# Performance work log

Measured on AMD Instinct MI355X. Metric: run time of the kernel, lower is better.

## Reference

```python
import jax, jax.numpy as jnp
import numpy as np


def setup_inputs() -> dict:
    key = jax.random.key(0)
    k1, k2 = jax.random.split(key)
    B, V = 8192, 32000
    outputs = jax.random.normal(k1, (B, V), dtype=jnp.float32)
    targets = jax.random.randint(k2, (B,), 0, V, dtype=jnp.int64)
    return {"outputs": outputs, "targets": targets}


def reference(outputs, targets):
    # stable log-softmax over vocab, then gather target log-prob per row
    logp = jax.nn.log_softmax(outputs, axis=-1)          # [B, V]
    picked = jnp.take_along_axis(logp, targets[:, None], axis=-1)[:, 0]  # [B]
    return -jnp.mean(picked)
```

## Files before the change

kernel.cpp:

```cpp
#include <hip/hip_runtime.h>
#include <math.h>


#define LOG2E 1.4426950408889634f
#define LN2   0.6931471805599453f

__global__ __launch_bounds__(256) void ce_row_kernel(const float* __restrict__ x,
                                                     const int* __restrict__ tgt,
                                                     float* __restrict__ row_loss,
                                                     int V) {
    const int row = blockIdx.x;
    const float* xr = x + (size_t)row * (size_t)V;
    const int tid = threadIdx.x;

    float m = -INFINITY;
    float s = 0.0f;
    const int nvec = V >> 2;
    const float4* __restrict__ xv = (const float4*)xr;

    for (int i = tid; i < nvec; i += 256) {
        float4 v = xv[i];
        float vm = fmaxf(fmaxf(v.x, v.y), fmaxf(v.z, v.w));
        float mn = fmaxf(m, vm);
        s = s * exp2f((m - mn) * LOG2E)
          + exp2f((v.x - mn) * LOG2E)
          + exp2f((v.y - mn) * LOG2E)
          + exp2f((v.z - mn) * LOG2E)
          + exp2f((v.w - mn) * LOG2E);
        m = mn;
    }

    #pragma unroll
    for (int off = 1; off < 64; off <<= 1) {
        float om = __shfl_xor(m, off);
        float os = __shfl_xor(s, off);
        float mn = fmaxf(m, om);
        s = s * exp2f((m - mn) * LOG2E) + os * exp2f((om - mn) * LOG2E);
        m = mn;
    }

    __shared__ float sm[4], ss[4];
    const int wave = tid >> 6;
    if ((tid & 63) == 0) { sm[wave] = m; ss[wave] = s; }
    __syncthreads();

    if (tid == 0) {
        float M = sm[0], S = ss[0];
        #pragma unroll
        for (int w = 1; w < 4; ++w) {
            float om = sm[w], os = ss[w];
            float mn = fmaxf(M, om);
            S = S * exp2f((M - mn) * LOG2E) + os * exp2f((om - mn) * LOG2E);
            M = mn;
        }
        float lse = M + log2f(S) * LN2;
        int t = tgt[row];
        row_loss[row] = lse - xr[t];
    }
}

__global__ __launch_bounds__(256) void ce_reduce_kernel(const float* __restrict__ row_loss,
                                                        float* __restrict__ out, int B) {
    float acc = 0.0f;
    for (int i = threadIdx.x; i < B; i += 256) acc += row_loss[i];
    #pragma unroll
    for (int off = 1; off < 64; off <<= 1) acc += __shfl_xor(acc, off);
    __shared__ float sa[4];
    if ((threadIdx.x & 63) == 0) sa[threadIdx.x >> 6] = acc;
    __syncthreads();
    if (threadIdx.x == 0) out[0] = (sa[0] + sa[1] + sa[2] + sa[3]) / (float)B;
}

extern "C" void kernel_launch(void* const* d_in, const int* in_sizes, int n_in,
                              void* d_out, int out_size, void* d_ws, size_t ws_size,
                              hipStream_t stream) {
    const float* x = (const float*)d_in[0];
    const int* tgt = (const int*)d_in[1];
    float* out = (float*)d_out;
    float* ws = (float*)d_ws;

    const int B = in_sizes[1];
    const int V = in_sizes[0] / B;

    ce_row_kernel<<<B, 256, 0, stream>>>(x, tgt, ws, V);
    ce_reduce_kernel<<<1, 256, 0, stream>>>(ws, out, B);
}
```

Before: 194.0 us.

## Map one wavefront per row and keep four independent online-softmax accumulators

```diff
diff --git a/kernel.cpp b/kernel.cpp
--- a/kernel.cpp
+++ b/kernel.cpp
@@ -8,54 +8,50 @@
 __global__ __launch_bounds__(256) void ce_row_kernel(const float* __restrict__ x,
                                                      const int* __restrict__ tgt,
                                                      float* __restrict__ row_loss,
-                                                     int V) {
-    const int row = blockIdx.x;
-    const float* xr = x + (size_t)row * (size_t)V;
-    const int tid = threadIdx.x;
+                                                     int V, int B) {
+    const int wave = threadIdx.x >> 6;
+    const int lane = threadIdx.x & 63;
+    const int row  = (blockIdx.x << 2) + wave;
+    if (row >= B) return;
 
-    float m = -INFINITY;
-    float s = 0.0f;
+    const float* __restrict__ xr = x + (size_t)row * (size_t)V;
+    const float4* __restrict__ xv = (const float4*)xr;
     const int nvec = V >> 2;
-    const float4* __restrict__ xv = (const float4*)xr;
 
-    for (int i = tid; i < nvec; i += 256) {
+    float m0 = -INFINITY, m1 = -INFINITY, m2 = -INFINITY, m3 = -INFINITY;
+    float s0 = 0.f, s1 = 0.f, s2 = 0.f, s3 = 0.f;
+
+    #pragma unroll 5
+    for (int i = lane; i < nvec; i += 64) {
         float4 v = xv[i];
-        float vm = fmaxf(fmaxf(v.x, v.y), fmaxf(v.z, v.w));
-        float mn = fmaxf(m, vm);
-        s = s * exp2f((m - mn) * LOG2E)
-          + exp2f((v.x - mn) * LOG2E)
-          + exp2f((v.y - mn) * LOG2E)
-          + exp2f((v.z - mn) * LOG2E)
-          + exp2f((v.w - mn) * LOG2E);
-        m = mn;
+        float w0 = v.x * LOG2E, w1 = v.y * LOG2E,
+              w2 = v.z * LOG2E, w3 = v.w * LOG2E;
+        float n0 = fmaxf(m0, w0);
+        s0 = s0 * exp2f(m0 - n0) + exp2f(w0 - n0); m0 = n0;
+        float n1 = fmaxf(m1, w1);
+        s1 = s1 * exp2f(m1 - n1) + exp2f(w1 - n1); m1 = n1;
+        float n2 = fmaxf(m2, w2);
+        s2 = s2 * exp2f(m2 - n2) + exp2f(w2 - n2); m2 = n2;
+        float n3 = fmaxf(m3, w3);
+        s3 = s3 * exp2f(m3 - n3) + exp2f(w3 - n3); m3 = n3;
     }
+
+    float M = fmaxf(fmaxf(m0, m1), fmaxf(m2, m3));
+    float S = s0 * exp2f(m0 - M) + s1 * exp2f(m1 - M)
+            + s2 * exp2f(m2 - M) + s3 * exp2f(m3 - M);
 
     #pragma unroll
     for (int off = 1; off < 64; off <<= 1) {
-        float om = __shfl_xor(m, off);
-        float os = __shfl_xor(s, off);
-        float mn = fmaxf(m, om);
-        s = s * exp2f((m - mn) * LOG2E) + os * exp2f((om - mn) * LOG2E);
-        m = mn;
+        float om = __shfl_xor(M, off);
+        float os = __shfl_xor(S, off);
+        float mn = fmaxf(M, om);
+        S = S * exp2f(M - mn) + os * exp2f(om - mn);
+        M = mn;
     }
 
-    __shared__ float sm[4], ss[4];
-    const int wave = tid >> 6;
-    if ((tid & 63) == 0) { sm[wave] = m; ss[wave] = s; }
-    __syncthreads();
-
-    if (tid == 0) {
-        float M = sm[0], S = ss[0];
-        #pragma unroll
-        for (int w = 1; w < 4; ++w) {
-            float om = sm[w], os = ss[w];
-            float mn = fmaxf(M, om);
-            S = S * exp2f((M - mn) * LOG2E) + os * exp2f((om - mn) * LOG2E);
-            M = mn;
-        }
-        float lse = M + log2f(S) * LN2;
-        int t = tgt[row];
-        row_loss[row] = lse - xr[t];
+    if (lane == 0) {
+        float lse = (M + log2f(S)) * LN2;
+        row_loss[row] = lse - xr[tgt[row]];
     }
 }
 
@@ -82,6 +78,6 @@
     const int B = in_sizes[1];
     const int V = in_sizes[0] / B;
 
-    ce_row_kernel<<<B, 256, 0, stream>>>(x, tgt, ws, V);
+    ce_row_kernel<<<(B + 3) / 4, 256, 0, stream>>>(x, tgt, ws, V, B);
     ce_reduce_kernel<<<1, 256, 0, stream>>>(ws, out, B);
 }
```

Measured after the change: 201.4 us. +3.8%, slower.
